# Kernel tuning notes

Measured on AMD Instinct MI355X. Metric: run time of the kernel, lower is better.

The kernel has to match this reference:

```python
import jax, jax.numpy as jnp
import numpy as np

B, C, H, W = 4, 64, 128, 128
G, K, PAD, DIL = 4, 3, 2, 2  # deformable conv config
OFF_CH = 2 * K * K * G  # 72


def conv2d(x, w, b, pad):
    out = jax.lax.conv_general_dilated(
        x, w, window_strides=(1, 1), padding=[(pad, pad), (pad, pad)],
        dimension_numbers=('NCHW', 'OIHW', 'NCHW'))
    return out + b[None, :, None, None]


def deform_conv(x, offset, w, b):
    # DCNv1 (no modulation mask), groups=G, offset_groups=G, torchvision semantics.
    Bn, Cn, Hn, Wn = x.shape
    Cg = Cn // G
    Cout = w.shape[0]
    Coutg = Cout // G
    # offset channels laid out as [G, K*K, (dy,dx)]
    off = offset.reshape(Bn, G, K * K, 2, Hn, Wn)
    dy, dx = off[:, :, :, 0], off[:, :, :, 1]  # [B,G,9,H,W]
    kk = jnp.arange(K * K)
    gy = (jnp.arange(Hn)[None, :] - PAD + DIL * (kk // K)[:, None]).astype(x.dtype)[:, :, None]  # [9,H,1]
    gx = (jnp.arange(Wn)[None, :] - PAD + DIL * (kk % K)[:, None]).astype(x.dtype)[:, None, :]   # [9,1,W]
    py = dy + gy[None, None]  # [B,G,9,H,W]
    px = dx + gx[None, None]
    xg = x.reshape(Bn, G, Cg, Hn, Wn)

    def gather(img, py_, px_):  # img [Cg,H,W]; py_,px_ [9,H,W]
        y0 = jnp.floor(py_)
        x0 = jnp.floor(px_)
        ly = py_ - y0
        lx = px_ - x0

        def corner(iy, ix, wgt):
            valid = (iy >= 0) & (iy <= Hn - 1) & (ix >= 0) & (ix <= Wn - 1)
            iyc = jnp.clip(iy, 0, Hn - 1).astype(jnp.int32)
            ixc = jnp.clip(ix, 0, Wn - 1).astype(jnp.int32)
            return img[:, iyc, ixc] * (wgt * valid)[None]

        return (corner(y0, x0, (1 - ly) * (1 - lx))
                + corner(y0, x0 + 1, (1 - ly) * lx)
                + corner(y0 + 1, x0, ly * (1 - lx))
                + corner(y0 + 1, x0 + 1, ly * lx))

    sampled = jax.vmap(jax.vmap(gather))(xg, py, px)  # [B,G,Cg,9,H,W]
    wr = w.reshape(G, Coutg, Cg, K * K)
    out = jnp.einsum('bgckhw,gock->bgohw', sampled, wr).reshape(Bn, Cout, Hn, Wn)
    return out + b[None, :, None, None]


def setup_inputs() -> dict:
    key = jax.random.key(0)
    ks = jax.random.split(key, 32)
    f32 = jnp.float32
    d = {
        'Fref': jax.random.normal(ks[0], (B, C, H, W), f32),
        'Fmov1': jax.random.normal(ks[1], (B, C, H, W), f32),
        'Fmov2': jax.random.normal(ks[2], (B, C, H, W), f32),
        'cr_w': jax.random.normal(ks[3], (64, 128, 3, 3), f32) * 0.05,
        'cr_b': jax.random.normal(ks[4], (64,), f32) * 0.05,
    }
    i = 5
    for name in ('off1', 'off2', 'off3', 'off4'):
        d[name + '_w'] = jax.random.normal(ks[i], (OFF_CH, 64, 3, 3), f32) * 0.01
        d[name + '_b'] = jax.random.normal(ks[i + 1], (OFF_CH,), f32) * 0.01
        i += 2
    for name in ('d1', 'd2', 'd3', 'd4'):
        d[name + '_w'] = jax.random.normal(ks[i], (64, 64 // G, 3, 3), f32) * 0.05
        d[name + '_b'] = jax.random.normal(ks[i + 1], (64,), f32) * 0.05
        i += 2
    return d


def reference(Fref, Fmov1, Fmov2, cr_w, cr_b,
              off1_w, off1_b, off2_w, off2_b, off3_w, off3_b, off4_w, off4_b,
              d1_w, d1_b, d2_w, d2_b, d3_w, d3_b, d4_w, d4_b):
    def align(fr, fm):
        fea = conv2d(jnp.concatenate([fr, fm], axis=1), cr_w, cr_b, 1)
        fea = deform_conv(fea, conv2d(fea, off1_w, off1_b, 1), d1_w, d1_b)
        fea = deform_conv(fea, conv2d(fea, off2_w, off2_b, 1), d2_w, d2_b)
        off3 = conv2d(fea, off3_w, off3_b, 1)
        fea = deform_conv(fm, off3, d3_w, d3_b)  # note: deform3 applied to Fmov, per source
        out = deform_conv(fea, conv2d(fea, off4_w, off4_b, 1), d4_w, d4_b)
        return out

    return (align(Fref, Fmov1), align(Fref, Fmov2))
```

## Files before the change

### kernel.cpp

```cpp
#include <hip/hip_runtime.h>


using f16   = _Float16;
using f16x8 = __attribute__((ext_vector_type(8))) f16;
using h2    = __attribute__((ext_vector_type(2))) f16;
using u16x8 = __attribute__((ext_vector_type(8))) unsigned short;
using f32x4 = __attribute__((ext_vector_type(4))) float;

static constexpr int Hh = 128, Ww = 128, NB = 4, NPIX = Hh * Ww;
static constexpr int BB = 8;

__device__ __forceinline__ unsigned short f2h(float f) {
  f16 h = (f16)f;
  return *(unsigned short*)&h;
}

struct PrepPtrs {
  const float* cw[5];
  unsigned short* cd[5];
  const float* dw[4];
  unsigned short* dd[4];
  const float* ob[4];
  float* obd[4];
};

__global__ __launch_bounds__(256) void prep_all_kernel(PrepPtrs pp) {
  const int which = blockIdx.y;
  const int i = blockIdx.x * 256 + threadIdx.x;
  if (which == 0) {
    if (i >= 9 * 64 * 128) return;
    const int cin = 128, cop = 64;
    const int ci = i % cin, co = (i / cin) % cop, t = i / (cin * cop);
    pp.cd[0][i] = f2h(pp.cw[0][((size_t)co * cin + ci) * 9 + t]);
  } else if (which <= 4) {
    if (i >= 9 * 80 * 64) return;
    const int cin = 64, cop = 80;
    const int ci = i % cin, co = (i / cin) % cop, t = i / (cin * cop);
    const int g = co / 20, c = co % 20;
    float v = (c < 18) ? pp.cw[which][((size_t)(g * 18 + c) * cin + ci) * 9 + t]
                       : 0.f;
    pp.cd[which][i] = f2h(v);
  } else if (which <= 8) {
    if (i >= 4 * 5 * 16 * 32) return;
    const int kk = i & 31, o = (i >> 5) & 15, pair = (i >> 9) % 5;
    const int g = i / 2560;
    const int t = pair * 2 + (kk >> 4), c = kk & 15;
    float v = (t < 9) ? pp.dw[which - 5][(size_t)((g * 16 + o) * 16 + c) * 9 + t]
                      : 0.f;
    pp.dd[which - 5][i] = f2h(v);
  } else {
    if (i >= 4 * 80) return;
    const int ten = i / 80, co = i % 80;
    const int g = co / 20, c = co % 20;
    pp.obd[ten][co] = (c < 18) ? pp.ob[ten][g * 18 + c] : 0.f;
  }
}

__global__ __launch_bounds__(256) void to_gs_kernel(
    const float* __restrict__ Fref, const float* __restrict__ Fm1,
    const float* __restrict__ Fm2, unsigned short* __restrict__ frefG,
    unsigned short* __restrict__ fmovG) {
  const int t = blockIdx.x * 256 + threadIdx.x;
  const int b2 = t >> 14, pix = t & (NPIX - 1);
  const float* fm = (b2 < 4 ? Fm1 : Fm2) + (size_t)(b2 & 3) * 64 * NPIX + pix;
  for (int c8 = 0; c8 < 8; ++c8) {
    u16x8 v;
#pragma unroll
    for (int j = 0; j < 8; ++j) v[j] = f2h(fm[(size_t)(c8 * 8 + j) * NPIX]);
    *(u16x8*)(fmovG + ((size_t)(b2 * 4 + (c8 >> 1)) * NPIX + pix) * 16 +
              (c8 & 1) * 8) = v;
  }
  if (b2 < 4) {
    const float* fr = Fref + (size_t)b2 * 64 * NPIX + pix;
    for (int c8 = 0; c8 < 8; ++c8) {
      u16x8 v;
#pragma unroll
      for (int j = 0; j < 8; ++j) v[j] = f2h(fr[(size_t)(c8 * 8 + j) * NPIX]);
      *(u16x8*)(frefG + ((size_t)(b2 * 4 + (c8 >> 1)) * NPIX + pix) * 16 +
                (c8 & 1) * 8) = v;
    }
  }
}

template <int CIN, int COP, int CO_REAL>
__global__ __launch_bounds__(512, 2) void convmfma_kernel(
    const unsigned short* __restrict__ in0, int bmask0,
    const unsigned short* __restrict__ in1, int bmask1,
    const unsigned short* __restrict__ wT,
    const float* __restrict__ biasP,
    unsigned short* __restrict__ out) {
  constexpr int COF = COP / 16;
  constexpr int NCH = CIN / 64;
  constexpr int NT = NCH * 9;
  __shared__ unsigned short sW[2][COP * 64];
  __shared__ unsigned short sB[324 * 64];

  const int tile = ((blockIdx.x & 7) << 3) | (blockIdx.x >> 3);
  const int b = blockIdx.y;
  const int ty0 = (tile >> 3) << 4, tx0 = (tile & 7) << 4;
  const int tid = threadIdx.x;
  const int wv = tid >> 6, l = tid & 63;
  const int lm = l & 15, lq = l >> 4;

  f32x4 acc[COF][2];
#pragma unroll
  for (int cf = 0; cf < COF; ++cf)
#pragma unroll
    for (int pf = 0; pf < 2; ++pf) acc[cf][pf] = (f32x4){0.f, 0.f, 0.f, 0.f};

  const unsigned short* base0 = in0 + (size_t)(b & bmask0) * 4 * NPIX * 16;
  const unsigned short* base1 =
      (NCH > 1) ? in1 + (size_t)(b & bmask1) * 4 * NPIX * 16 : nullptr;

  auto stage_input = [&](int ch) {
    const unsigned short* inB = (ch == 0) ? base0 : base1;
    for (int q = tid; q < 324 * 8; q += 512) {
      const int pix = q >> 3, ci8 = q & 7;
      const int r = pix / 18, c = pix - r * 18;
      const int gy = ty0 - 1 + r, gx = tx0 - 1 + c;
      u16x8 v;
      if (gy >= 0 && gy < Hh && gx >= 0 && gx < Ww) {
        v = *(const u16x8*)(inB + ((size_t)(ci8 >> 1) * NPIX + gy * Ww + gx) *
                                      16 + (ci8 & 1) * 8);
      } else {
#pragma unroll
        for (int j = 0; j < 8; ++j) v[j] = 0;
      }
      const int boff = pix * 128 + ((ci8 * 16) ^ ((pix & 7) << 4));
      *(u16x8*)((char*)sB + boff) = v;
    }
  };
  auto stage_w = [&](int tt, int buf) {
    const int ch = tt / 9, t = tt - ch * 9;
    for (int q = tid; q < COP * 8; q += 512) {
      const int ci8 = q & 7;
      const int co = q >> 3;
      u16x8 v = *(const u16x8*)(wT + (size_t)(t * COP + co) * CIN + ch * 64 +
                                ci8 * 8);
      const int aoff = co * 128 + ((ci8 * 16) ^ ((co & 7) << 4));
      *(u16x8*)((char*)sW[buf] + aoff) = v;
    }
  };

  stage_input(0);
  stage_w(0, 0);
  __syncthreads();

  for (int tt = 0; tt < NT; ++tt) {
    const int t = tt % 9;
    const bool nextNewCh = ((tt + 1) % 9 == 0);
    if (tt + 1 < NT && !nextNewCh) stage_w(tt + 1, (tt + 1) & 1);

    const int dy = t / 3, dx = t - dy * 3;
    const char* sWc = (const char*)sW[tt & 1];
#pragma unroll
    for (int kc = 0; kc < 2; ++kc) {
      f16x8 afr[COF];
#pragma unroll
      for (int cf = 0; cf < COF; ++cf) {
        const int co = cf * 16 + lm;
        const int aoff = co * 128 + ((kc * 64 + lq * 16) ^ ((co & 7) << 4));
        afr[cf] = *(const f16x8*)(sWc + aoff);
      }
#pragma unroll
      for (int pf = 0; pf < 2; ++pf) {
        const int pix = wv * 32 + pf * 16 + lm;
        const int spix = ((pix >> 4) + dy) * 18 + (pix & 15) + dx;
        const int boff = spix * 128 + ((kc * 64 + lq * 16) ^ ((spix & 7) << 4));
        const f16x8 bfr = *(const f16x8*)((const char*)sB + boff);
#pragma unroll
        for (int cf = 0; cf < COF; ++cf)
          acc[cf][pf] = __builtin_amdgcn_mfma_f32_16x16x32_f16(
              afr[cf], bfr, acc[cf][pf], 0, 0, 0);
      }
    }
    __syncthreads();
    if (tt + 1 < NT && nextNewCh) {
      stage_input((tt + 1) / 9);
      stage_w(tt + 1, (tt + 1) & 1);
      __syncthreads();
    }
  }

#pragma unroll
  for (int cf = 0; cf < COF; ++cf) {
    const int co0 = cf * 16 + lq * 4;
    if (co0 >= CO_REAL) continue;
    const float4 bv = *(const float4*)(biasP + co0);
#pragma unroll
    for (int pf = 0; pf < 2; ++pf) {
      const int pix = wv * 32 + pf * 16 + lm;
      const int gpix = (ty0 + (pix >> 4)) * Ww + tx0 + (pix & 15);
      const f32x4 v = acc[cf][pf];
      ushort4 pk;
      pk.x = f2h(v[0] + bv.x);
      pk.y = f2h(v[1] + bv.y);
      pk.z = f2h(v[2] + bv.z);
      pk.w = f2h(v[3] + bv.w);
      const int gg = co0 >> 4, cc = co0 & 15;
      *(ushort4*)(out + ((size_t)(b * 4 + gg) * NPIX + gpix) * 16 + cc) = pk;
    }
  }
}

template <bool NCHW_OUT>
__global__ __launch_bounds__(256, 4) void fused_od_kernel(
    const unsigned short* __restrict__ convIn,
    const unsigned short* __restrict__ sampX,
    const unsigned short* __restrict__ wT,
    const float* __restrict__ obias,
    const unsigned short* __restrict__ dwP,
    const float* __restrict__ dbias,
    float* __restrict__ outF, unsigned short* __restrict__ outH) {
  __shared__ __attribute__((aligned(16))) char lds[36352];
  char* sB = lds;
  char* sW = lds + 26112;
  char* sOffB = lds;
  char* bounce = lds + 26112;

  const int tile = ((blockIdx.x & 7) << 4) | (blockIdx.x >> 3);
  const int b = blockIdx.y;
  const int ty0 = (tile >> 2) << 2;
  const int tx0 = (tile & 3) << 5;
  const int tid = threadIdx.x;
  const int wv = tid >> 6, l = tid & 63;
  const int lm = l & 15, lq = l >> 4;

  f32x4 acc[5][2];
#pragma unroll
  for (int cf = 0; cf < 5; ++cf)
#pragma unroll
    for (int pf = 0; pf < 2; ++pf) acc[cf][pf] = (f32x4){0.f, 0.f, 0.f, 0.f};

  const unsigned short* inB = convIn + (size_t)b * 4 * NPIX * 16;

  u16x8 wr0, wr1, wr2;
  auto wload = [&](int t) {
    const unsigned short* wt = wT + (size_t)t * 5120;
    wr0 = *(const u16x8*)(wt + (size_t)(tid >> 3) * 64 + (tid & 7) * 8);
    const int q1 = tid + 256;
    wr1 = *(const u16x8*)(wt + (size_t)(q1 >> 3) * 64 + (q1 & 7) * 8);
    if (tid < 128) {
      const int q2 = tid + 512;
      wr2 = *(const u16x8*)(wt + (size_t)(q2 >> 3) * 64 + (q2 & 7) * 8);
    }
  };
  auto wstore = [&]() {
    auto put = [&](int q, u16x8 v) {
      const int co = q >> 3, ci8 = q & 7;
      *(u16x8*)(sW + co * 128 + ((ci8 * 16) ^ ((co & 7) << 4))) = v;
    };
    put(tid, wr0);
    put(tid + 256, wr1);
    if (tid < 128) put(tid + 512, wr2);
  };

  wload(0);
  for (int q = tid; q < 204 * 8; q += 256) {
    const int pix = q >> 3, ci8 = q & 7;
    const int r = pix / 34, c = pix - r * 34;
    const int gy = ty0 - 1 + r, gx = tx0 - 1 + c;
    u16x8 v;
    if (gy >= 0 && gy < Hh && gx >= 0 && gx < Ww) {
      v = *(const u16x8*)(inB + ((size_t)(ci8 >> 1) * NPIX + gy * Ww + gx) *
                                    16 + (ci8 & 1) * 8);
    } else {
#pragma unroll
      for (int j = 0; j < 8; ++j) v[j] = 0;
    }
    const int boff = pix * 128 + ((ci8 * 16) ^ ((pix & 7) << 4));
    *(u16x8*)(sB + boff) = v;
  }
  wstore();
  __syncthreads();

  for (int t = 0; t < 9; ++t) {
    if (t + 1 < 9) wload(t + 1);
    const int dy = t / 3, dx = t - dy * 3;
#pragma unroll
    for (int kc = 0; kc < 2; ++kc) {
      f16x8 afr[5];
#pragma unroll
      for (int cf = 0; cf < 5; ++cf) {
        const int co = cf * 16 + lm;
        const int aoff = co * 128 + ((kc * 64 + lq * 16) ^ ((co & 7) << 4));
        afr[cf] = *(const f16x8*)(sW + aoff);
      }
#pragma unroll
      for (int pf = 0; pf < 2; ++pf) {
        const int pix = wv * 32 + pf * 16 + lm;
        const int spix = ((pix >> 5) + dy) * 34 + (pix & 31) + dx;
        const int boff = spix * 128 + ((kc * 64 + lq * 16) ^ ((spix & 7) << 4));
        const f16x8 bfr = *(const f16x8*)(sB + boff);
#pragma unroll
        for (int cf = 0; cf < 5; ++cf)
          acc[cf][pf] = __builtin_amdgcn_mfma_f32_16x16x32_f16(
              afr[cf], bfr, acc[cf][pf], 0, 0, 0);
      }
    }
    __syncthreads();
    if (t + 1 < 9) {
      wstore();
      __syncthreads();
    }
  }

#pragma unroll
  for (int cf = 0; cf < 5; ++cf) {
    const int co0 = cf * 16 + lq * 4;
    const float4 bv = *(const float4*)(obias + co0);
#pragma unroll
    for (int pf = 0; pf < 2; ++pf) {
      const int pix = wv * 32 + pf * 16 + lm;
      const f32x4 v = acc[cf][pf];
      ushort4 pk;
      pk.x = f2h(v[0] + bv.x);
      pk.y = f2h(v[1] + bv.y);
      pk.z = f2h(v[2] + bv.z);
      pk.w = f2h(v[3] + bv.w);
      *(ushort4*)(sOffB + pix * 168 + co0 * 2) = pk;
    }
  }
  __syncthreads();

  const int p = tid >> 1, h = tid & 1;
  const int y = ty0 + (p >> 5), xx = tx0 + (p & 31);
  char* myB = bounce + p * 80 + h * 16;

  for (int g = 0; g < 4; ++g) {
    const unsigned short* xP =
        sampX + (size_t)(b * 4 + g) * NPIX * 16 + h * 8;
    unsigned od[9];
#pragma unroll
    for (int t = 0; t < 9; ++t)
      od[t] = *(const unsigned*)(sOffB + p * 168 + (g * 20 + 2 * t) * 2);

    f16x8 afr[5];
#pragma unroll
    for (int pr = 0; pr < 5; ++pr)
      afr[pr] = *(const f16x8*)(dwP + ((size_t)(g * 5 + pr) * 16 + lm) * 32 +
                                lq * 8);

    f32x4 dacc[2];
    dacc[0] = (f32x4){0.f, 0.f, 0.f, 0.f};
    dacc[1] = (f32x4){0.f, 0.f, 0.f, 0.f};

#pragma unroll
    for (int pair = 0; pair < 5; ++pair) {
#pragma unroll
      for (int ti = 0; ti < 2; ++ti) {
        const int t = pair * 2 + ti;
        uint4 sv = (uint4){0u, 0u, 0u, 0u};
        if (t < 9) {
          const unsigned odw = od[t];
          const f16* op = (const f16*)&odw;
          const float dy = (float)op[0];
          const float dx = (float)op[1];
          const float py = dy + (float)(y - 2 + 2 * (t / 3));
          const float px = dx + (float)(xx - 2 + 2 * (t % 3));
          const float fy = floorf(py), fx = floorf(px);
          const int y0 = (int)fy, x0 = (int)fx;
          const int y1 = y0 + 1, x1 = x0 + 1;
          const float ly = py - fy, lx = px - fx;
          float w00 = (1.f - ly) * (1.f - lx), w01 = (1.f - ly) * lx;
          float w10 = ly * (1.f - lx), w11 = ly * lx;
          const bool vy0 = (y0 >= 0) && (y0 < Hh), vy1 = (y1 >= 0) && (y1 < Hh);
          const bool vx0 = (x0 >= 0) && (x0 < Ww), vx1 = (x1 >= 0) && (x1 < Ww);
          w00 = (vy0 && vx0) ? w00 : 0.f;
          w01 = (vy0 && vx1) ? w01 : 0.f;
          w10 = (vy1 && vx0) ? w10 : 0.f;
          w11 = (vy1 && vx1) ? w11 : 0.f;
          const int y0c = min(max(y0, 0), Hh - 1), y1c = min(max(y1, 0), Hh - 1);
          const int x0c = min(max(x0, 0), Ww - 1), x1c = min(max(x1, 0), Ww - 1);
          const u16x8 a00 = *(const u16x8*)(xP + (size_t)(y0c * Ww + x0c) * 16);
          const u16x8 a01 = *(const u16x8*)(xP + (size_t)(y0c * Ww + x1c) * 16);
          const u16x8 a10 = *(const u16x8*)(xP + (size_t)(y1c * Ww + x0c) * 16);
          const u16x8 a11 = *(const u16x8*)(xP + (size_t)(y1c * Ww + x1c) * 16);
          const h2* c00 = (const h2*)&a00;
          const h2* c01 = (const h2*)&a01;
          const h2* c10 = (const h2*)&a10;
          const h2* c11 = (const h2*)&a11;
          const f16 h00 = (f16)w00, h01 = (f16)w01;
          const f16 h10 = (f16)w10, h11 = (f16)w11;
          const h2 p00 = (h2){h00, h00}, p01 = (h2){h01, h01};
          const h2 p10 = (h2){h10, h10}, p11 = (h2){h11, h11};
          unsigned fw[4];
#pragma unroll
          for (int j = 0; j < 4; ++j) {
            h2 r = c00[j] * p00;
            r += c01[j] * p01;
            r += c10[j] * p10;
            r += c11[j] * p11;
            fw[j] = *(const unsigned*)&r;
          }
          sv = (uint4){fw[0], fw[1], fw[2], fw[3]};
        }
        *(uint4*)(myB + ti * 32) = sv;
      }
#pragma unroll
      for (int n = 0; n < 2; ++n) {
        const f16x8 bfr =
            *(const f16x8*)(bounce + (wv * 32 + n * 16 + lm) * 80 + lq * 16);
        dacc[n] = __builtin_amdgcn_mfma_f32_16x16x32_f16(afr[pair], bfr,
                                                         dacc[n], 0, 0, 0);
      }
    }

    const float4 bv = *(const float4*)(dbias + g * 16 + lq * 4);
#pragma unroll
    for (int n = 0; n < 2; ++n) {
      const int pixl = wv * 32 + n * 16 + lm;
      const int gpix = (ty0 + (pixl >> 5)) * Ww + tx0 + (pixl & 31);
      const f32x4 v = dacc[n];
      if (NCHW_OUT) {
        float* oB = outF + (size_t)(b * 64 + g * 16 + lq * 4) * NPIX + gpix;
        oB[0] = v[0] + bv.x;
        oB[NPIX] = v[1] + bv.y;
        oB[2 * NPIX] = v[2] + bv.z;
        oB[3 * NPIX] = v[3] + bv.w;
      } else {
        ushort4 pk;
        pk.x = f2h(v[0] + bv.x);
        pk.y = f2h(v[1] + bv.y);
        pk.z = f2h(v[2] + bv.z);
        pk.w = f2h(v[3] + bv.w);
        *(ushort4*)(outH + ((size_t)(b * 4 + g) * NPIX + gpix) * 16 + lq * 4) =
            pk;
      }
    }
  }
}


extern "C" void kernel_launch(void* const* d_in, const int* in_sizes, int n_in,
                              void* d_out, int out_size, void* d_ws,
                              size_t ws_size, hipStream_t stream) {
  const float* Fref = (const float*)d_in[0];
  const float* Fmov1 = (const float*)d_in[1];
  const float* Fmov2 = (const float*)d_in[2];
  const float* cr_w = (const float*)d_in[3];
  const float* cr_b = (const float*)d_in[4];
  const float* offw[4] = {(const float*)d_in[5], (const float*)d_in[7],
                          (const float*)d_in[9], (const float*)d_in[11]};
  const float* offb[4] = {(const float*)d_in[6], (const float*)d_in[8],
                          (const float*)d_in[10], (const float*)d_in[12]};
  const float* dw[4] = {(const float*)d_in[13], (const float*)d_in[15],
                        (const float*)d_in[17], (const float*)d_in[19]};
  const float* db[4] = {(const float*)d_in[14], (const float*)d_in[16],
                        (const float*)d_in[18], (const float*)d_in[20]};

  char* p = (char*)d_ws;
  auto carve = [&](size_t bytes) {
    void* r = p;
    p += (bytes + 255) & ~(size_t)255;
    return r;
  };
  unsigned short* frefG = (unsigned short*)carve((size_t)4 * 4 * NPIX * 16 * 2);
  unsigned short* fmovG = (unsigned short*)carve((size_t)BB * 4 * NPIX * 16 * 2);
  unsigned short* feaA = (unsigned short*)carve((size_t)BB * 4 * NPIX * 16 * 2);
  unsigned short* feaB = (unsigned short*)carve((size_t)BB * 4 * NPIX * 16 * 2);
  unsigned short* wcrT = (unsigned short*)carve((size_t)9 * 64 * 128 * 2);
  unsigned short* woffT[4];
  for (int i = 0; i < 4; ++i)
    woffT[i] = (unsigned short*)carve((size_t)9 * 80 * 64 * 2);
  unsigned short* dwP[4];
  for (int i = 0; i < 4; ++i)
    dwP[i] = (unsigned short*)carve((size_t)4 * 5 * 16 * 32 * 2);
  float* obP[4];
  for (int i = 0; i < 4; ++i) obP[i] = (float*)carve((size_t)80 * 4);

  PrepPtrs pp;
  pp.cw[0] = cr_w;
  pp.cd[0] = wcrT;
  for (int i = 0; i < 4; ++i) {
    pp.cw[i + 1] = offw[i];
    pp.cd[i + 1] = woffT[i];
    pp.dw[i] = dw[i];
    pp.dd[i] = dwP[i];
    pp.ob[i] = offb[i];
    pp.obd[i] = obP[i];
  }
  prep_all_kernel<<<dim3(288, 10), 256, 0, stream>>>(pp);

  to_gs_kernel<<<BB * NPIX / 256, 256, 0, stream>>>(Fref, Fmov1, Fmov2, frefG,
                                                    fmovG);

  const dim3 cgrid(64, BB), cblk(512);
  const dim3 fgrid(128, BB), fblk(256);
  float* outF = (float*)d_out;

  convmfma_kernel<128, 64, 64><<<cgrid, cblk, 0, stream>>>(
      frefG, 3, fmovG, 7, wcrT, cr_b, feaA);
  fused_od_kernel<false><<<fgrid, fblk, 0, stream>>>(
      feaA, feaA, woffT[0], obP[0], dwP[0], db[0], nullptr, feaB);
  fused_od_kernel<false><<<fgrid, fblk, 0, stream>>>(
      feaB, feaB, woffT[1], obP[1], dwP[1], db[1], nullptr, feaA);
  fused_od_kernel<false><<<fgrid, fblk, 0, stream>>>(
      feaA, fmovG, woffT[2], obP[2], dwP[2], db[2], nullptr, feaB);
  fused_od_kernel<true><<<fgrid, fblk, 0, stream>>>(
      feaB, feaB, woffT[3], obP[3], dwP[3], db[3], outF, nullptr);
}
```

Measured before the change: 229.0 us.

## Software-pipeline bilinear gather loads in fused offset/deform kernel

Restructures the deformable sampling loop so the four corner gathers for the next tap are issued before the current tap is blended. Two register slots double-buffer the loaded corner vectors and weights, and offsets are read from LDS on demand. The goal is to hide global/L2 gather latency behind the blend ALU work. Launch bounds drop from 4 to 3 waves per SIMD to make room for the extra live registers, at some cost in occupancy. Tap 9 is now computed with zero weight instead of being skipped, which adds some redundant loads.

Result: no change. 224.7 us (-1.9%).

```diff
diff --git a/kernel.cpp b/kernel.cpp
--- a/kernel.cpp
+++ b/kernel.cpp
@@ -204,7 +204,7 @@
 }
 
 template <bool NCHW_OUT>
-__global__ __launch_bounds__(256, 4) void fused_od_kernel(
+__global__ __launch_bounds__(256, 3) void fused_od_kernel(
     const unsigned short* __restrict__ convIn,
     const unsigned short* __restrict__ sampX,
     const unsigned short* __restrict__ wT,
@@ -330,10 +330,6 @@
   for (int g = 0; g < 4; ++g) {
     const unsigned short* xP =
         sampX + (size_t)(b * 4 + g) * NPIX * 16 + h * 8;
-    unsigned od[9];
-#pragma unroll
-    for (int t = 0; t < 9; ++t)
-      od[t] = *(const unsigned*)(sOffB + p * 168 + (g * 20 + 2 * t) * 2);
 
     f16x8 afr[5];
 #pragma unroll
@@ -345,58 +341,73 @@
     dacc[0] = (f32x4){0.f, 0.f, 0.f, 0.f};
     dacc[1] = (f32x4){0.f, 0.f, 0.f, 0.f};
 
+    u16x8 ld[2][4];
+    f16 wgt[2][4];
+
+    auto prefetch = [&](int t, int slot) {
+      float dyo = 0.f, dxo = 0.f;
+      if (t < 9) {
+        const unsigned odw =
+            *(const unsigned*)(sOffB + p * 168 + (g * 20 + 2 * t) * 2);
+        const f16* op = (const f16*)&odw;
+        dyo = (float)op[0];
+        dxo = (float)op[1];
+      }
+      const int tc = (t < 9) ? t : 0;
+      const float act = (t < 9) ? 1.f : 0.f;
+      const float py = dyo + (float)(y - 2 + 2 * (tc / 3));
+      const float px = dxo + (float)(xx - 2 + 2 * (tc % 3));
+      const float fy = floorf(py), fx = floorf(px);
+      const int y0 = (int)fy, x0 = (int)fx;
+      const int y1 = y0 + 1, x1 = x0 + 1;
+      const float ly = py - fy, lx = px - fx;
+      float w00 = (1.f - ly) * (1.f - lx) * act, w01 = (1.f - ly) * lx * act;
+      float w10 = ly * (1.f - lx) * act, w11 = ly * lx * act;
+      const bool vy0 = (y0 >= 0) && (y0 < Hh), vy1 = (y1 >= 0) && (y1 < Hh);
+      const bool vx0 = (x0 >= 0) && (x0 < Ww), vx1 = (x1 >= 0) && (x1 < Ww);
+      w00 = (vy0 && vx0) ? w00 : 0.f;
+      w01 = (vy0 && vx1) ? w01 : 0.f;
+      w10 = (vy1 && vx0) ? w10 : 0.f;
+      w11 = (vy1 && vx1) ? w11 : 0.f;
+      const int y0c = min(max(y0, 0), Hh - 1), y1c = min(max(y1, 0), Hh - 1);
+      const int x0c = min(max(x0, 0), Ww - 1), x1c = min(max(x1, 0), Ww - 1);
+      ld[slot][0] = *(const u16x8*)(xP + (size_t)(y0c * Ww + x0c) * 16);
+      ld[slot][1] = *(const u16x8*)(xP + (size_t)(y0c * Ww + x1c) * 16);
+      ld[slot][2] = *(const u16x8*)(xP + (size_t)(y1c * Ww + x0c) * 16);
+      ld[slot][3] = *(const u16x8*)(xP + (size_t)(y1c * Ww + x1c) * 16);
+      wgt[slot][0] = (f16)w00;
+      wgt[slot][1] = (f16)w01;
+      wgt[slot][2] = (f16)w10;
+      wgt[slot][3] = (f16)w11;
+    };
+    auto consume = [&](int slot, char* dst) {
+      const h2* c00 = (const h2*)&ld[slot][0];
+      const h2* c01 = (const h2*)&ld[slot][1];
+      const h2* c10 = (const h2*)&ld[slot][2];
+      const h2* c11 = (const h2*)&ld[slot][3];
+      const h2 p00 = (h2){wgt[slot][0], wgt[slot][0]};
+      const h2 p01 = (h2){wgt[slot][1], wgt[slot][1]};
+      const h2 p10 = (h2){wgt[slot][2], wgt[slot][2]};
+      const h2 p11 = (h2){wgt[slot][3], wgt[slot][3]};
+      unsigned fw[4];
+#pragma unroll
+      for (int j = 0; j < 4; ++j) {
+        h2 r = c00[j] * p00;
+        r += c01[j] * p01;
+        r += c10[j] * p10;
+        r += c11[j] * p11;
+        fw[j] = *(const unsigned*)&r;
+      }
+      *(uint4*)dst = (uint4){fw[0], fw[1], fw[2], fw[3]};
+    };
+
+    prefetch(0, 0);
 #pragma unroll
     for (int pair = 0; pair < 5; ++pair) {
-#pragma unroll
-      for (int ti = 0; ti < 2; ++ti) {
-        const int t = pair * 2 + ti;
-        uint4 sv = (uint4){0u, 0u, 0u, 0u};
-        if (t < 9) {
-          const unsigned odw = od[t];
-          const f16* op = (const f16*)&odw;
-          const float dy = (float)op[0];
-          const float dx = (float)op[1];
-          const float py = dy + (float)(y - 2 + 2 * (t / 3));
-          const float px = dx + (float)(xx - 2 + 2 * (t % 3));
-          const float fy = floorf(py), fx = floorf(px);
-          const int y0 = (int)fy, x0 = (int)fx;
-          const int y1 = y0 + 1, x1 = x0 + 1;
-          const float ly = py - fy, lx = px - fx;
-          float w00 = (1.f - ly) * (1.f - lx), w01 = (1.f - ly) * lx;
-          float w10 = ly * (1.f - lx), w11 = ly * lx;
-          const bool vy0 = (y0 >= 0) && (y0 < Hh), vy1 = (y1 >= 0) && (y1 < Hh);
-          const bool vx0 = (x0 >= 0) && (x0 < Ww), vx1 = (x1 >= 0) && (x1 < Ww);
-          w00 = (vy0 && vx0) ? w00 : 0.f;
-          w01 = (vy0 && vx1) ? w01 : 0.f;
-          w10 = (vy1 && vx0) ? w10 : 0.f;
-          w11 = (vy1 && vx1) ? w11 : 0.f;
-          const int y0c = min(max(y0, 0), Hh - 1), y1c = min(max(y1, 0), Hh - 1);
-          const int x0c = min(max(x0, 0), Ww - 1), x1c = min(max(x1, 0), Ww - 1);
-          const u16x8 a00 = *(const u16x8*)(xP + (size_t)(y0c * Ww + x0c) * 16);
-          const u16x8 a01 = *(const u16x8*)(xP + (size_t)(y0c * Ww + x1c) * 16);
-          const u16x8 a10 = *(const u16x8*)(xP + (size_t)(y1c * Ww + x0c) * 16);
-          const u16x8 a11 = *(const u16x8*)(xP + (size_t)(y1c * Ww + x1c) * 16);
-          const h2* c00 = (const h2*)&a00;
-          const h2* c01 = (const h2*)&a01;
-          const h2* c10 = (const h2*)&a10;
-          const h2* c11 = (const h2*)&a11;
-          const f16 h00 = (f16)w00, h01 = (f16)w01;
-          const f16 h10 = (f16)w10, h11 = (f16)w11;
-          const h2 p00 = (h2){h00, h00}, p01 = (h2){h01, h01};
-          const h2 p10 = (h2){h10, h10}, p11 = (h2){h11, h11};
-          unsigned fw[4];
-#pragma unroll
-          for (int j = 0; j < 4; ++j) {
-            h2 r = c00[j] * p00;
-            r += c01[j] * p01;
-            r += c10[j] * p10;
-            r += c11[j] * p11;
-            fw[j] = *(const unsigned*)&r;
-          }
-          sv = (uint4){fw[0], fw[1], fw[2], fw[3]};
-        }
-        *(uint4*)(myB + ti * 32) = sv;
-      }
+      prefetch(pair * 2 + 1, 1);
+      consume(0, myB);
+      if (pair < 4) prefetch(pair * 2 + 2, 0);
+      consume(1, myB + 32);
 #pragma unroll
       for (int n = 0; n < 2; ++n) {
         const f16x8 bfr =
```
